# Kernel optimization log

Measured on AMD Instinct MI355X. Metric: run time of the kernel, lower is better.

The kernel has to match this reference:

```python
import jax, jax.numpy as jnp
import numpy as np

N_NODES = 50000
N_EDGES = 800000
N_GRAPHS = 256
IN_CH = 128
DIM = 128
OUT_CH = 2


def _gcn_conv(x, W, b, src, dst, n_nodes):
    # PyG GCNConv: add self-loops, symmetric normalization D^-1/2 (A+I) D^-1/2, then XW + b
    h = x @ W  # [N, dim]
    deg = jax.ops.segment_sum(jnp.ones((src.shape[0],), h.dtype), dst, num_segments=n_nodes) + 1.0
    dinv = jax.lax.rsqrt(deg)  # deg >= 1 due to self loop
    norm = dinv[src] * dinv[dst]  # [E]
    agg = jax.ops.segment_sum(h[src] * norm[:, None], dst, num_segments=n_nodes)
    agg = agg + h * (dinv * dinv)[:, None]  # self-loop contribution
    return agg + b


def _mean_pool(x, batch, n_graphs):
    s = jax.ops.segment_sum(x, batch, num_segments=n_graphs)
    cnt = jax.ops.segment_sum(jnp.ones((x.shape[0],), x.dtype), batch, num_segments=n_graphs)
    return s / jnp.maximum(cnt, 1.0)[:, None]


def setup_inputs() -> dict:
    key = jax.random.key(0)
    ks = jax.random.split(key, 12)
    x = jax.random.normal(ks[0], (N_NODES, IN_CH), dtype=jnp.float32)
    edge_index = jax.random.randint(ks[1], (2, N_EDGES), 0, N_NODES, dtype=jnp.int64)
    batch = jnp.sort(jax.random.randint(ks[2], (N_NODES,), 0, N_GRAPHS, dtype=jnp.int64))
    def glorot(k, shape):
        lim = np.sqrt(6.0 / (shape[0] + shape[1]))
        return jax.random.uniform(k, shape, jnp.float32, -lim, lim)
    return {
        "x": x,
        "edge_index": edge_index,
        "batch": batch,
        "W1": glorot(ks[3], (IN_CH, DIM)),
        "b1": jnp.zeros((DIM,), jnp.float32),
        "W2": glorot(ks[4], (DIM, DIM)),
        "b2": jnp.zeros((DIM,), jnp.float32),
        "L1W": glorot(ks[5], (2 * DIM, DIM)),
        "L1b": jnp.zeros((DIM,), jnp.float32),
        "L2W": glorot(ks[6], (DIM, OUT_CH)),
        "L2b": jnp.zeros((OUT_CH,), jnp.float32),
    }


def reference(x, edge_index, batch, W1, b1, W2, b2, L1W, L1b, L2W, L2b):
    src, dst = edge_index[0], edge_index[1]
    n = x.shape[0]
    h1 = jax.nn.relu(_gcn_conv(x, W1, b1, src, dst, n))
    p1 = _mean_pool(h1, batch, N_GRAPHS)
    h2 = jax.nn.relu(_gcn_conv(h1, W2, b2, src, dst, n))
    p2 = _mean_pool(h2, batch, N_GRAPHS)
    g = jnp.concatenate([p1, p2], axis=-1)  # JK cat -> [G, 2*dim]
    g = jax.nn.relu(g @ L1W + L1b)
    # dropout is identity in eval mode
    out = g @ L2W + L2b
    return jax.nn.log_softmax(out, axis=-1)
```

## Files before the change

kernel.cpp:

```cpp
#include <hip/hip_runtime.h>

#define N_NODES 50000
#define N_EDGES 800000
#define N_GRAPHS 256
#define DIM 128

#define NBUCK 196
#define A_BLOCKS 200
#define A_EPB 4000
#define N_SEG (NBUCK * A_BLOCKS)
#define SCANA_B 1024
#define SCANA_NB 39

typedef __attribute__((ext_vector_type(8))) short bf16x8;
typedef __attribute__((ext_vector_type(4))) float f32x4;
typedef __attribute__((ext_vector_type(8))) unsigned short u16x8;

__device__ __forceinline__ unsigned short f2bf(float f) {
    union { float f; unsigned u; } v; v.f = f;
    unsigned u = v.u;
    u += 0x7fffu + ((u >> 16) & 1u);
    return (unsigned short)(u >> 16);
}
__device__ __forceinline__ float bf2f(unsigned short h) {
    union { unsigned u; float f; } v; v.u = ((unsigned)h) << 16;
    return v.f;
}

__global__ __launch_bounds__(256) void a1_count_kernel(const int* __restrict__ dst,
                                                       int* __restrict__ cntA) {
    __shared__ int hist[NBUCK];
    int t = threadIdx.x;
    for (int b = t; b < NBUCK; b += 256) hist[b] = 0;
    __syncthreads();
    int base = blockIdx.x * A_EPB;
    for (int i = t; i < A_EPB; i += 256) {
        int d = dst[base + i];
        atomicAdd(&hist[d >> 8], 1);
    }
    __syncthreads();
    for (int b = t; b < NBUCK; b += 256) cntA[b * A_BLOCKS + blockIdx.x] = hist[b];
}

__global__ __launch_bounds__(SCANA_B) void reduceN_kernel(const int* __restrict__ in,
                                                          int* __restrict__ bsum) {
    __shared__ int red[SCANA_B / 64];
    int idx = blockIdx.x * SCANA_B + threadIdx.x;
    int v = (idx < N_SEG) ? in[idx] : 0;
    for (int d = 32; d >= 1; d >>= 1) v += __shfl_down(v, d, 64);
    if ((threadIdx.x & 63) == 0) red[threadIdx.x >> 6] = v;
    __syncthreads();
    if (threadIdx.x == 0) {
        int s = 0;
        for (int w = 0; w < SCANA_B / 64; ++w) s += red[w];
        bsum[blockIdx.x] = s;
    }
}

__global__ __launch_bounds__(64) void scanblkN_kernel(int* __restrict__ bsum) {
    if (threadIdx.x == 0) {
        int run = 0;
        for (int i = 0; i < SCANA_NB; ++i) { int c = bsum[i]; bsum[i] = run; run += c; }
    }
}

__global__ __launch_bounds__(SCANA_B) void scanoutN_kernel(const int* __restrict__ in,
                                                           const int* __restrict__ boff,
                                                           int* __restrict__ outx) {
    __shared__ int s[SCANA_B];
    int t = threadIdx.x;
    int idx = blockIdx.x * SCANA_B + t;
    int c = (idx < N_SEG) ? in[idx] : 0;
    s[t] = c;
    __syncthreads();
    for (int d = 1; d < SCANA_B; d <<= 1) {
        int v = s[t];
        if (t >= d) v += s[t - d];
        __syncthreads();
        s[t] = v;
        __syncthreads();
    }
    if (idx < N_SEG) outx[idx] = boff[blockIdx.x] + s[t] - c;
}

__global__ __launch_bounds__(256) void a2_scatter_kernel(const int* __restrict__ src,
                                                         const int* __restrict__ dst,
                                                         const int* __restrict__ baseA,
                                                         int2* __restrict__ ebuf) {
    __shared__ int cur[NBUCK];
    int t = threadIdx.x;
    for (int b = t; b < NBUCK; b += 256) cur[b] = baseA[b * A_BLOCKS + blockIdx.x];
    __syncthreads();
    int base = blockIdx.x * A_EPB;
    for (int i = t; i < A_EPB; i += 256) {
        int e = base + i;
        int sN = src[e], d = dst[e];
        int pos = atomicAdd(&cur[d >> 8], 1);
        int2 r; r.x = sN; r.y = d;
        ebuf[pos] = r;
    }
}

__global__ __launch_bounds__(512) void bucket_kernel(const int2* __restrict__ ebuf,
                                                     const int* __restrict__ baseA,
                                                     int2* __restrict__ sedge,
                                                     int* __restrict__ rowptr,
                                                     float* __restrict__ dinv) {
    int b = blockIdx.x;
    int t = threadIdx.x;
    __shared__ int cnt[256], sc[256], cur[256];
    __shared__ int se[2];
    if (t == 0) {
        se[0] = baseA[b * A_BLOCKS];
        se[1] = (b + 1 < NBUCK) ? baseA[(b + 1) * A_BLOCKS] : N_EDGES;
    }
    if (t < 256) cnt[t] = 0;
    __syncthreads();
    int start = se[0], end = se[1];
    for (int i = start + t; i < end; i += 512) atomicAdd(&cnt[ebuf[i].y & 255], 1);
    __syncthreads();
    if (t < 256) sc[t] = cnt[t];
    __syncthreads();
    for (int d = 1; d < 256; d <<= 1) {
        int v = 0;
        if (t < 256) { v = sc[t]; if (t >= d) v += sc[t - d]; }
        __syncthreads();
        if (t < 256) sc[t] = v;
        __syncthreads();
    }
    if (t < 256) {
        int excl = start + sc[t] - cnt[t];
        cur[t] = excl;
        int v = b * 256 + t;
        if (v < N_NODES) {
            rowptr[v] = excl;
            dinv[v] = rsqrtf((float)(cnt[t] + 1));
        }
    }
    if (b == 0 && t == 0) rowptr[N_NODES] = N_EDGES;
    __syncthreads();
    for (int i = start + t; i < end; i += 512) {
        int2 r = ebuf[i];
        int pos = atomicAdd(&cur[r.y & 255], 1);
        sedge[pos] = r;
    }
}

__global__ __launch_bounds__(512) void weight_kernel(int2* __restrict__ sedge,
                                                     const float* __restrict__ dinv) {
    int i = blockIdx.x * 512 + threadIdx.x;
    if (i < N_EDGES) {
        int2 r = sedge[i];
        float w = dinv[r.x] * dinv[r.y];
        r.y = __float_as_int(w);
        sedge[i] = r;
    }
}

#define LDK 136
__global__ __launch_bounds__(256) void mm_mfma_kernel(const float* __restrict__ X,
                                                      const float* __restrict__ W,
                                                      unsigned short* __restrict__ Y,
                                                      int nrows) {
    __shared__ __align__(16) unsigned short Xs[128 * LDK];
    __shared__ __align__(16) unsigned short Wt[128 * LDK];
    int t = threadIdx.x;

    for (int idx = t; idx < 128 * 128; idx += 256) {
        int k = idx >> 7, c = idx & 127;
        Wt[c * LDK + k] = f2bf(W[idx]);
    }
    int r0 = blockIdx.x * 128;
    const float4* X4 = (const float4*)X;
    for (int idx = t; idx < 128 * 32; idx += 256) {
        int r = idx >> 5, q = idx & 31;
        int gr = r0 + r;
        float4 vv = (gr < nrows) ? X4[(size_t)gr * 32 + q] : make_float4(0.f, 0.f, 0.f, 0.f);
        int base = r * LDK + q * 4;
        Xs[base + 0] = f2bf(vv.x);
        Xs[base + 1] = f2bf(vv.y);
        Xs[base + 2] = f2bf(vv.z);
        Xs[base + 3] = f2bf(vv.w);
    }
    __syncthreads();

    int w  = t >> 6;
    int l  = t & 63;
    int lg = l >> 4;
    int lr = l & 15;

    f32x4 acc[2][8];
#pragma unroll
    for (int rs = 0; rs < 2; ++rs)
#pragma unroll
        for (int cs = 0; cs < 8; ++cs) acc[rs][cs] = (f32x4){0.f, 0.f, 0.f, 0.f};

#pragma unroll
    for (int ks = 0; ks < 4; ++ks) {
        int koff = ks * 32 + lg * 8;
        bf16x8 a0 = *(const bf16x8*)&Xs[(w * 32 + 0 + lr) * LDK + koff];
        bf16x8 a1 = *(const bf16x8*)&Xs[(w * 32 + 16 + lr) * LDK + koff];
#pragma unroll
        for (int cs = 0; cs < 8; ++cs) {
            bf16x8 b = *(const bf16x8*)&Wt[(cs * 16 + lr) * LDK + koff];
            acc[0][cs] = __builtin_amdgcn_mfma_f32_16x16x32_bf16(a0, b, acc[0][cs], 0, 0, 0);
            acc[1][cs] = __builtin_amdgcn_mfma_f32_16x16x32_bf16(a1, b, acc[1][cs], 0, 0, 0);
        }
    }

#pragma unroll
    for (int rs = 0; rs < 2; ++rs) {
        int rbase = r0 + w * 32 + rs * 16 + lg * 4;
#pragma unroll
        for (int cs = 0; cs < 8; ++cs) {
            int c = cs * 16 + lr;
#pragma unroll
            for (int reg = 0; reg < 4; ++reg) {
                int r = rbase + reg;
                if (r < nrows) Y[(size_t)r * 128 + c] = f2bf(acc[rs][cs][reg]);
            }
        }
    }
}

__global__ __launch_bounds__(256) void agg_kernel(const unsigned short* __restrict__ Hbf,
                                                  const int* __restrict__ rowptr,
                                                  const int2* __restrict__ sedge,
                                                  const float* __restrict__ dinv,
                                                  const float* __restrict__ bias,
                                                  float* __restrict__ O) {
    int gw = (int)((blockIdx.x * 256 + threadIdx.x) >> 6);
    if (gw >= N_NODES) return;
    int v = __builtin_amdgcn_readfirstlane(gw);
    int lane = threadIdx.x & 63;
    int q = lane >> 4;
    int f = lane & 15;
    const u16x8* H8 = (const u16x8*)Hbf;
    float a0 = 0.f, a1 = 0.f, a2 = 0.f, a3 = 0.f,
          a4 = 0.f, a5 = 0.f, a6 = 0.f, a7 = 0.f;
    int e0 = rowptr[v], eend = rowptr[v + 1];
    for (int base = e0; base < eend; base += 16) {
#pragma unroll
        for (int k = 0; k < 4; ++k) {
            int ee = base + 4 * k + q;
            bool inb = ee < eend;
            int ec = inb ? ee : e0;
            int2 rec = sedge[ec];
            int s = rec.x;
            float w = inb ? __int_as_float(rec.y) : 0.f;
            u16x8 h = H8[(size_t)s * 16 + f];
            a0 += w * bf2f(h[0]);
            a1 += w * bf2f(h[1]);
            a2 += w * bf2f(h[2]);
            a3 += w * bf2f(h[3]);
            a4 += w * bf2f(h[4]);
            a5 += w * bf2f(h[5]);
            a6 += w * bf2f(h[6]);
            a7 += w * bf2f(h[7]);
        }
    }
    a0 += __shfl_xor(a0, 16, 64); a0 += __shfl_xor(a0, 32, 64);
    a1 += __shfl_xor(a1, 16, 64); a1 += __shfl_xor(a1, 32, 64);
    a2 += __shfl_xor(a2, 16, 64); a2 += __shfl_xor(a2, 32, 64);
    a3 += __shfl_xor(a3, 16, 64); a3 += __shfl_xor(a3, 32, 64);
    a4 += __shfl_xor(a4, 16, 64); a4 += __shfl_xor(a4, 32, 64);
    a5 += __shfl_xor(a5, 16, 64); a5 += __shfl_xor(a5, 32, 64);
    a6 += __shfl_xor(a6, 16, 64); a6 += __shfl_xor(a6, 32, 64);
    a7 += __shfl_xor(a7, 16, 64); a7 += __shfl_xor(a7, 32, 64);
    if (q == 0) {
        float dv = dinv[v];
        float sc = dv * dv;
        u16x8 hs = H8[(size_t)v * 16 + f];
        float4 b4a = ((const float4*)bias)[f * 2 + 0];
        float4 b4b = ((const float4*)bias)[f * 2 + 1];
        float4 oa, ob;
        oa.x = fmaxf(a0 + sc * bf2f(hs[0]) + b4a.x, 0.f);
        oa.y = fmaxf(a1 + sc * bf2f(hs[1]) + b4a.y, 0.f);
        oa.z = fmaxf(a2 + sc * bf2f(hs[2]) + b4a.z, 0.f);
        oa.w = fmaxf(a3 + sc * bf2f(hs[3]) + b4a.w, 0.f);
        ob.x = fmaxf(a4 + sc * bf2f(hs[4]) + b4b.x, 0.f);
        ob.y = fmaxf(a5 + sc * bf2f(hs[5]) + b4b.y, 0.f);
        ob.z = fmaxf(a6 + sc * bf2f(hs[6]) + b4b.z, 0.f);
        ob.w = fmaxf(a7 + sc * bf2f(hs[7]) + b4b.w, 0.f);
        float4* O4 = (float4*)O;
        O4[(size_t)v * 32 + f * 2 + 0] = oa;
        O4[(size_t)v * 32 + f * 2 + 1] = ob;
    }
}

__device__ __forceinline__ int lbound(const int* __restrict__ a, int n, int v) {
    int lo = 0, hi = n;
    while (lo < hi) {
        int mid = (lo + hi) >> 1;
        if (a[mid] < v) lo = mid + 1; else hi = mid;
    }
    return lo;
}

__global__ __launch_bounds__(512) void pool_kernel(const float* __restrict__ H,
                                                   const int* __restrict__ batch,
                                                   float* __restrict__ P) {
    int g = blockIdx.x;
    __shared__ int sse[2];
    __shared__ float red[512];
    if (threadIdx.x < 2) sse[threadIdx.x] = lbound(batch, N_NODES, g + threadIdx.x);
    __syncthreads();
    int ss = sse[0], se = sse[1];
    int d = threadIdx.x & 127, c = threadIdx.x >> 7;
    float sum = 0.f;
    for (int n = ss + c; n < se; n += 4) sum += H[(size_t)n * 128 + d];
    red[threadIdx.x] = sum;
    __syncthreads();
    if (threadIdx.x < 128) {
        float s = red[threadIdx.x] + red[threadIdx.x + 128] + red[threadIdx.x + 256] + red[threadIdx.x + 384];
        float cntf = (float)(se - ss);
        P[g * 128 + threadIdx.x] = s / fmaxf(cntf, 1.f);
    }
}

__global__ __launch_bounds__(128) void mlp_kernel(const float* __restrict__ P1,
                                                  const float* __restrict__ P2,
                                                  const float* __restrict__ L1W,
                                                  const float* __restrict__ L1b,
                                                  const float* __restrict__ L2W,
                                                  const float* __restrict__ L2b,
                                                  float* __restrict__ out) {
    int g = blockIdx.x, j = threadIdx.x;
    __shared__ float gv[256];
    __shared__ float hid[128];
    gv[j] = P1[g * 128 + j];
    gv[128 + j] = P2[g * 128 + j];
    __syncthreads();
    float acc = L1b[j];
#pragma unroll 8
    for (int k = 0; k < 256; ++k) acc = fmaf(gv[k], L1W[k * 128 + j], acc);
    hid[j] = fmaxf(acc, 0.f);
    __syncthreads();
    if (j == 0) {
        float o0 = L2b[0], o1 = L2b[1];
        for (int k = 0; k < 128; ++k) {
            o0 += hid[k] * L2W[2 * k + 0];
            o1 += hid[k] * L2W[2 * k + 1];
        }
        float m = fmaxf(o0, o1);
        float lse = m + logf(expf(o0 - m) + expf(o1 - m));
        out[g * 2 + 0] = o0 - lse;
        out[g * 2 + 1] = o1 - lse;
    }
}

extern "C" void kernel_launch(void* const* d_in, const int* in_sizes, int n_in,
                              void* d_out, int out_size, void* d_ws, size_t ws_size,
                              hipStream_t stream) {
    const float* x    = (const float*)d_in[0];
    const int*   ei   = (const int*)d_in[1];
    const int*   batch= (const int*)d_in[2];
    const float* W1   = (const float*)d_in[3];
    const float* b1   = (const float*)d_in[4];
    const float* W2   = (const float*)d_in[5];
    const float* b2   = (const float*)d_in[6];
    const float* L1W  = (const float*)d_in[7];
    const float* L1b  = (const float*)d_in[8];
    const float* L2W  = (const float*)d_in[9];
    const float* L2b  = (const float*)d_in[10];
    float* out = (float*)d_out;

    const int* e_src = ei;
    const int* e_dst = ei + N_EDGES;

    char* ws = (char*)d_ws;
    size_t off = 0;
    auto alloc = [&](size_t bytes) {
        void* p = ws + off;
        off += (bytes + 255) & ~(size_t)255;
        return p;
    };
    int*   cntA      = (int*)alloc((size_t)N_SEG * 4);
    int*   bsumA     = (int*)alloc(SCANA_NB * 4);
    int*   baseA     = (int*)alloc((size_t)N_SEG * 4);
    int2*  ebuf      = (int2*)alloc((size_t)N_EDGES * 8);
    int2*  sedge     = (int2*)alloc((size_t)N_EDGES * 8);
    int*   rowptr    = (int*)alloc((N_NODES + 1) * 4);
    float* dinv      = (float*)alloc(N_NODES * 4);
    float* p1        = (float*)alloc(N_GRAPHS * DIM * 4);
    float* p2        = (float*)alloc(N_GRAPHS * DIM * 4);
    unsigned short* bufBf = (unsigned short*)alloc((size_t)N_NODES * DIM * 2);
    float* bufB      = (float*)alloc((size_t)N_NODES * DIM * 4);
    (void)ws_size; (void)in_sizes; (void)n_in; (void)out_size;

    a1_count_kernel<<<A_BLOCKS, 256, 0, stream>>>(e_dst, cntA);
    reduceN_kernel<<<SCANA_NB, SCANA_B, 0, stream>>>(cntA, bsumA);
    scanblkN_kernel<<<1, 64, 0, stream>>>(bsumA);
    scanoutN_kernel<<<SCANA_NB, SCANA_B, 0, stream>>>(cntA, bsumA, baseA);
    a2_scatter_kernel<<<A_BLOCKS, 256, 0, stream>>>(e_src, e_dst, baseA, ebuf);
    bucket_kernel<<<NBUCK, 512, 0, stream>>>(ebuf, baseA, sedge, rowptr, dinv);
    weight_kernel<<<(N_EDGES + 511) / 512, 512, 0, stream>>>(sedge, dinv);

    const int MMB = (N_NODES + 127) / 128;
    const int AGB = (N_NODES * 64 + 255) / 256;

    mm_mfma_kernel<<<MMB, 256, 0, stream>>>(x, W1, bufBf, N_NODES);
    agg_kernel<<<AGB, 256, 0, stream>>>(bufBf, rowptr, sedge, dinv, b1, bufB);
    pool_kernel<<<N_GRAPHS, 512, 0, stream>>>(bufB, batch, p1);

    mm_mfma_kernel<<<MMB, 256, 0, stream>>>(bufB, W2, bufBf, N_NODES);
    agg_kernel<<<AGB, 256, 0, stream>>>(bufBf, rowptr, sedge, dinv, b2, bufB);
    pool_kernel<<<N_GRAPHS, 512, 0, stream>>>(bufB, batch, p2);

    mlp_kernel<<<N_GRAPHS, 128, 0, stream>>>(p1, p2, L1W, L1b, L2W, L2b, out);
}
```

Before: 275.0 us.

## Store layer activations in bf16 and fold block-offset scan into scan kernel

The aggregation output is now written as bf16 instead of fp32. Pooling and the second matmul read this bf16 buffer directly, with vectorized 16-byte loads. This halves activation traffic across agg, pool and mm and drops the fp32-to-bf16 conversion in the second matmul. The serial block-sum scan kernel is removed; each scan block instead reduces the preceding block sums itself, saving one launch. Rounding the ReLU outputs to bf16 adds a little numerical error in the pooled features.

Measured after the change: 252.6 us. -8.1%, faster.

```diff
diff --git a/kernel.cpp b/kernel.cpp
--- a/kernel.cpp
+++ b/kernel.cpp
@@ -57,18 +57,17 @@
     }
 }
 
-__global__ __launch_bounds__(64) void scanblkN_kernel(int* __restrict__ bsum) {
-    if (threadIdx.x == 0) {
-        int run = 0;
-        for (int i = 0; i < SCANA_NB; ++i) { int c = bsum[i]; bsum[i] = run; run += c; }
-    }
-}
-
 __global__ __launch_bounds__(SCANA_B) void scanoutN_kernel(const int* __restrict__ in,
-                                                           const int* __restrict__ boff,
+                                                           const int* __restrict__ bsum,
                                                            int* __restrict__ outx) {
     __shared__ int s[SCANA_B];
-    int t = threadIdx.x;
+    __shared__ int boffs;
+    int t = threadIdx.x;
+    if (t < 64) {
+        int v = (t < blockIdx.x) ? bsum[t] : 0;
+        for (int d = 32; d >= 1; d >>= 1) v += __shfl_down(v, d, 64);
+        if (t == 0) boffs = v;
+    }
     int idx = blockIdx.x * SCANA_B + t;
     int c = (idx < N_SEG) ? in[idx] : 0;
     s[t] = c;
@@ -80,7 +79,7 @@
         s[t] = v;
         __syncthreads();
     }
-    if (idx < N_SEG) outx[idx] = boff[blockIdx.x] + s[t] - c;
+    if (idx < N_SEG) outx[idx] = boffs + s[t] - c;
 }
 
 __global__ __launch_bounds__(256) void a2_scatter_kernel(const int* __restrict__ src,
@@ -158,14 +157,54 @@
 }
 
 #define LDK 136
-__global__ __launch_bounds__(256) void mm_mfma_kernel(const float* __restrict__ X,
-                                                      const float* __restrict__ W,
-                                                      unsigned short* __restrict__ Y,
-                                                      int nrows) {
+__device__ __forceinline__ void mm_core(const unsigned short* Xs, const unsigned short* Wt,
+                                        unsigned short* __restrict__ Y, int r0, int nrows, int t) {
+    int w  = t >> 6;
+    int l  = t & 63;
+    int lg = l >> 4;
+    int lr = l & 15;
+
+    f32x4 acc[2][8];
+#pragma unroll
+    for (int rs = 0; rs < 2; ++rs)
+#pragma unroll
+        for (int cs = 0; cs < 8; ++cs) acc[rs][cs] = (f32x4){0.f, 0.f, 0.f, 0.f};
+
+#pragma unroll
+    for (int ks = 0; ks < 4; ++ks) {
+        int koff = ks * 32 + lg * 8;
+        bf16x8 a0 = *(const bf16x8*)&Xs[(w * 32 + 0 + lr) * LDK + koff];
+        bf16x8 a1 = *(const bf16x8*)&Xs[(w * 32 + 16 + lr) * LDK + koff];
+#pragma unroll
+        for (int cs = 0; cs < 8; ++cs) {
+            bf16x8 b = *(const bf16x8*)&Wt[(cs * 16 + lr) * LDK + koff];
+            acc[0][cs] = __builtin_amdgcn_mfma_f32_16x16x32_bf16(a0, b, acc[0][cs], 0, 0, 0);
+            acc[1][cs] = __builtin_amdgcn_mfma_f32_16x16x32_bf16(a1, b, acc[1][cs], 0, 0, 0);
+        }
+    }
+
+#pragma unroll
+    for (int rs = 0; rs < 2; ++rs) {
+        int rbase = r0 + w * 32 + rs * 16 + lg * 4;
+#pragma unroll
+        for (int cs = 0; cs < 8; ++cs) {
+            int c = cs * 16 + lr;
+#pragma unroll
+            for (int reg = 0; reg < 4; ++reg) {
+                int r = rbase + reg;
+                if (r < nrows) Y[(size_t)r * 128 + c] = f2bf(acc[rs][cs][reg]);
+            }
+        }
+    }
+}
+
+__global__ __launch_bounds__(256) void mm_mfma_f32_kernel(const float* __restrict__ X,
+                                                          const float* __restrict__ W,
+                                                          unsigned short* __restrict__ Y,
+                                                          int nrows) {
     __shared__ __align__(16) unsigned short Xs[128 * LDK];
     __shared__ __align__(16) unsigned short Wt[128 * LDK];
     int t = threadIdx.x;
-
     for (int idx = t; idx < 128 * 128; idx += 256) {
         int k = idx >> 7, c = idx & 127;
         Wt[c * LDK + k] = f2bf(W[idx]);
@@ -183,44 +222,31 @@
         Xs[base + 3] = f2bf(vv.w);
     }
     __syncthreads();
-
-    int w  = t >> 6;
-    int l  = t & 63;
-    int lg = l >> 4;
-    int lr = l & 15;
-
-    f32x4 acc[2][8];
-#pragma unroll
-    for (int rs = 0; rs < 2; ++rs)
-#pragma unroll
-        for (int cs = 0; cs < 8; ++cs) acc[rs][cs] = (f32x4){0.f, 0.f, 0.f, 0.f};
-
-#pragma unroll
-    for (int ks = 0; ks < 4; ++ks) {
-        int koff = ks * 32 + lg * 8;
-        bf16x8 a0 = *(const bf16x8*)&Xs[(w * 32 + 0 + lr) * LDK + koff];
-        bf16x8 a1 = *(const bf16x8*)&Xs[(w * 32 + 16 + lr) * LDK + koff];
-#pragma unroll
-        for (int cs = 0; cs < 8; ++cs) {
-            bf16x8 b = *(const bf16x8*)&Wt[(cs * 16 + lr) * LDK + koff];
-            acc[0][cs] = __builtin_amdgcn_mfma_f32_16x16x32_bf16(a0, b, acc[0][cs], 0, 0, 0);
-            acc[1][cs] = __builtin_amdgcn_mfma_f32_16x16x32_bf16(a1, b, acc[1][cs], 0, 0, 0);
-        }
-    }
-
-#pragma unroll
-    for (int rs = 0; rs < 2; ++rs) {
-        int rbase = r0 + w * 32 + rs * 16 + lg * 4;
-#pragma unroll
-        for (int cs = 0; cs < 8; ++cs) {
-            int c = cs * 16 + lr;
-#pragma unroll
-            for (int reg = 0; reg < 4; ++reg) {
-                int r = rbase + reg;
-                if (r < nrows) Y[(size_t)r * 128 + c] = f2bf(acc[rs][cs][reg]);
-            }
-        }
-    }
+    mm_core(Xs, Wt, Y, r0, nrows, t);
+}
+
+__global__ __launch_bounds__(256) void mm_mfma_bf16_kernel(const unsigned short* __restrict__ X,
+                                                           const float* __restrict__ W,
+                                                           unsigned short* __restrict__ Y,
+                                                           int nrows) {
+    __shared__ __align__(16) unsigned short Xs[128 * LDK];
+    __shared__ __align__(16) unsigned short Wt[128 * LDK];
+    int t = threadIdx.x;
+    for (int idx = t; idx < 128 * 128; idx += 256) {
+        int k = idx >> 7, c = idx & 127;
+        Wt[c * LDK + k] = f2bf(W[idx]);
+    }
+    int r0 = blockIdx.x * 128;
+    const u16x8* X8 = (const u16x8*)X;
+    u16x8 z = {0, 0, 0, 0, 0, 0, 0, 0};
+    for (int idx = t; idx < 128 * 16; idx += 256) {
+        int r = idx >> 4, q = idx & 15;
+        int gr = r0 + r;
+        u16x8 vv = (gr < nrows) ? X8[(size_t)gr * 16 + q] : z;
+        *(u16x8*)&Xs[r * LDK + q * 8] = vv;
+    }
+    __syncthreads();
+    mm_core(Xs, Wt, Y, r0, nrows, t);
 }
 
 __global__ __launch_bounds__(256) void agg_kernel(const unsigned short* __restrict__ Hbf,
@@ -228,7 +254,7 @@
                                                   const int2* __restrict__ sedge,
                                                   const float* __restrict__ dinv,
                                                   const float* __restrict__ bias,
-                                                  float* __restrict__ O) {
+                                                  unsigned short* __restrict__ O) {
     int gw = (int)((blockIdx.x * 256 + threadIdx.x) >> 6);
     if (gw >= N_NODES) return;
     int v = __builtin_amdgcn_readfirstlane(gw);
@@ -273,18 +299,16 @@
         u16x8 hs = H8[(size_t)v * 16 + f];
         float4 b4a = ((const float4*)bias)[f * 2 + 0];
         float4 b4b = ((const float4*)bias)[f * 2 + 1];
-        float4 oa, ob;
-        oa.x = fmaxf(a0 + sc * bf2f(hs[0]) + b4a.x, 0.f);
-        oa.y = fmaxf(a1 + sc * bf2f(hs[1]) + b4a.y, 0.f);
-        oa.z = fmaxf(a2 + sc * bf2f(hs[2]) + b4a.z, 0.f);
-        oa.w = fmaxf(a3 + sc * bf2f(hs[3]) + b4a.w, 0.f);
-        ob.x = fmaxf(a4 + sc * bf2f(hs[4]) + b4b.x, 0.f);
-        ob.y = fmaxf(a5 + sc * bf2f(hs[5]) + b4b.y, 0.f);
-        ob.z = fmaxf(a6 + sc * bf2f(hs[6]) + b4b.z, 0.f);
-        ob.w = fmaxf(a7 + sc * bf2f(hs[7]) + b4b.w, 0.f);
-        float4* O4 = (float4*)O;
-        O4[(size_t)v * 32 + f * 2 + 0] = oa;
-        O4[(size_t)v * 32 + f * 2 + 1] = ob;
+        u16x8 o;
+        o[0] = f2bf(fmaxf(a0 + sc * bf2f(hs[0]) + b4a.x, 0.f));
+        o[1] = f2bf(fmaxf(a1 + sc * bf2f(hs[1]) + b4a.y, 0.f));
+        o[2] = f2bf(fmaxf(a2 + sc * bf2f(hs[2]) + b4a.z, 0.f));
+        o[3] = f2bf(fmaxf(a3 + sc * bf2f(hs[3]) + b4a.w, 0.f));
+        o[4] = f2bf(fmaxf(a4 + sc * bf2f(hs[4]) + b4b.x, 0.f));
+        o[5] = f2bf(fmaxf(a5 + sc * bf2f(hs[5]) + b4b.y, 0.f));
+        o[6] = f2bf(fmaxf(a6 + sc * bf2f(hs[6]) + b4b.z, 0.f));
+        o[7] = f2bf(fmaxf(a7 + sc * bf2f(hs[7]) + b4b.w, 0.f));
+        ((u16x8*)O)[(size_t)v * 16 + f] = o;
     }
 }
 
@@ -297,24 +321,33 @@
     return lo;
 }
 
-__global__ __launch_bounds__(512) void pool_kernel(const float* __restrict__ H,
+__global__ __launch_bounds__(512) void pool_kernel(const unsigned short* __restrict__ H,
                                                    const int* __restrict__ batch,
                                                    float* __restrict__ P) {
     int g = blockIdx.x;
     __shared__ int sse[2];
-    __shared__ float red[512];
-    if (threadIdx.x < 2) sse[threadIdx.x] = lbound(batch, N_NODES, g + threadIdx.x);
+    __shared__ float red[32][129];
+    int t = threadIdx.x;
+    if (t < 2) sse[t] = lbound(batch, N_NODES, g + t);
     __syncthreads();
     int ss = sse[0], se = sse[1];
-    int d = threadIdx.x & 127, c = threadIdx.x >> 7;
-    float sum = 0.f;
-    for (int n = ss + c; n < se; n += 4) sum += H[(size_t)n * 128 + d];
-    red[threadIdx.x] = sum;
-    __syncthreads();
-    if (threadIdx.x < 128) {
-        float s = red[threadIdx.x] + red[threadIdx.x + 128] + red[threadIdx.x + 256] + red[threadIdx.x + 384];
+    int f = t & 15, c = t >> 4;
+    const u16x8* H8 = (const u16x8*)H;
+    float a[8] = {0.f, 0.f, 0.f, 0.f, 0.f, 0.f, 0.f, 0.f};
+    for (int n = ss + c; n < se; n += 32) {
+        u16x8 h = H8[(size_t)n * 16 + f];
+#pragma unroll
+        for (int k = 0; k < 8; ++k) a[k] += bf2f(h[k]);
+    }
+#pragma unroll
+    for (int k = 0; k < 8; ++k) red[c][f * 8 + k] = a[k];
+    __syncthreads();
+    if (t < 128) {
+        float s = 0.f;
+#pragma unroll 8
+        for (int c2 = 0; c2 < 32; ++c2) s += red[c2][t];
         float cntf = (float)(se - ss);
-        P[g * 128 + threadIdx.x] = s / fmaxf(cntf, 1.f);
+        P[g * 128 + t] = s / fmaxf(cntf, 1.f);
     }
 }
 
@@ -385,12 +418,11 @@
     float* p1        = (float*)alloc(N_GRAPHS * DIM * 4);
     float* p2        = (float*)alloc(N_GRAPHS * DIM * 4);
     unsigned short* bufBf = (unsigned short*)alloc((size_t)N_NODES * DIM * 2);
-    float* bufB      = (float*)alloc((size_t)N_NODES * DIM * 4);
+    unsigned short* bufH  = (unsigned short*)alloc((size_t)N_NODES * DIM * 2);
     (void)ws_size; (void)in_sizes; (void)n_in; (void)out_size;
 
     a1_count_kernel<<<A_BLOCKS, 256, 0, stream>>>(e_dst, cntA);
     reduceN_kernel<<<SCANA_NB, SCANA_B, 0, stream>>>(cntA, bsumA);
-    scanblkN_kernel<<<1, 64, 0, stream>>>(bsumA);
     scanoutN_kernel<<<SCANA_NB, SCANA_B, 0, stream>>>(cntA, bsumA, baseA);
     a2_scatter_kernel<<<A_BLOCKS, 256, 0, stream>>>(e_src, e_dst, baseA, ebuf);
     bucket_kernel<<<NBUCK, 512, 0, stream>>>(ebuf, baseA, sedge, rowptr, dinv);
@@ -399,13 +431,13 @@
     const int MMB = (N_NODES + 127) / 128;
     const int AGB = (N_NODES * 64 + 255) / 256;
 
-    mm_mfma_kernel<<<MMB, 256, 0, stream>>>(x, W1, bufBf, N_NODES);
-    agg_kernel<<<AGB, 256, 0, stream>>>(bufBf, rowptr, sedge, dinv, b1, bufB);
-    pool_kernel<<<N_GRAPHS, 512, 0, stream>>>(bufB, batch, p1);
-
-    mm_mfma_kernel<<<MMB, 256, 0, stream>>>(bufB, W2, bufBf, N_NODES);
-    agg_kernel<<<AGB, 256, 0, stream>>>(bufBf, rowptr, sedge, dinv, b2, bufB);
-    pool_kernel<<<N_GRAPHS, 512, 0, stream>>>(bufB, batch, p2);
+    mm_mfma_f32_kernel<<<MMB, 256, 0, stream>>>(x, W1, bufBf, N_NODES);
+    agg_kernel<<<AGB, 256, 0, stream>>>(bufBf, rowptr, sedge, dinv, b1, bufH);
+    pool_kernel<<<N_GRAPHS, 512, 0, stream>>>(bufH, batch, p1);
+
+    mm_mfma_bf16_kernel<<<MMB, 256, 0, stream>>>(bufH, W2, bufBf, N_NODES);
+    agg_kernel<<<AGB, 256, 0, stream>>>(bufBf, rowptr, sedge, dinv, b2, bufH);
+    pool_kernel<<<N_GRAPHS, 512, 0, stream>>>(bufH, batch, p2);
 
     mlp_kernel<<<N_GRAPHS, 128, 0, stream>>>(p1, p2, L1W, L1b, L2W, L2b, out);
 }
```
